# Kernel tuning notes

Hardware: AMD Instinct MI355X
Metric: run time of the kernel (lower is better)

## Reference

```python
import jax, jax.numpy as jnp
import numpy as np

N_NODES = 50000
N_EDGES = 800000
DIM = 128
N_LAYERS = 2          # num_layers - 1 GIN layers
NUM_GRAPHS = 512      # rows of the sparse graph_pool matrix
BN_EPS = 1e-5


def setup_inputs() -> dict:
    key = jax.random.key(0)
    ks = jax.random.split(key, 10)
    x = jax.random.normal(ks[0], (N_NODES, DIM), dtype=jnp.float32)
    edge_src = jax.random.randint(ks[1], (N_EDGES,), 0, N_NODES, dtype=jnp.int32)
    edge_dst = jax.random.randint(ks[2], (N_EDGES,), 0, N_NODES, dtype=jnp.int32)
    edge_weight = jax.random.uniform(ks[3], (N_EDGES,), dtype=jnp.float32)
    graph_ids = jnp.sort(jax.random.randint(ks[4], (N_NODES,), 0, NUM_GRAPHS, dtype=jnp.int32))
    pool_w = jnp.ones((N_NODES,), dtype=jnp.float32)
    scale = 1.0 / np.sqrt(DIM)
    W1 = jax.random.normal(ks[5], (N_LAYERS, DIM, DIM), dtype=jnp.float32) * scale
    b1 = jnp.zeros((N_LAYERS, DIM), dtype=jnp.float32)
    W2 = jax.random.normal(ks[6], (N_LAYERS, DIM, DIM), dtype=jnp.float32) * scale
    b2 = jnp.zeros((N_LAYERS, DIM), dtype=jnp.float32)
    bn_gamma = jnp.ones((N_LAYERS, DIM), dtype=jnp.float32)
    bn_beta = jnp.zeros((N_LAYERS, DIM), dtype=jnp.float32)
    return {"x": x, "edge_src": edge_src, "edge_dst": edge_dst,
            "edge_weight": edge_weight, "graph_ids": graph_ids, "pool_w": pool_w,
            "W1": W1, "b1": b1, "W2": W2, "b2": b2,
            "bn_gamma": bn_gamma, "bn_beta": bn_beta}


def reference(x, edge_src, edge_dst, edge_weight, graph_ids, pool_w,
              W1, b1, W2, b2, bn_gamma, bn_beta):
    h = x
    n = h.shape[0]
    for l in range(N_LAYERS):
        # pooled = adj @ h, adj in COO form: adj[dst, src] = edge_weight
        msg = edge_weight[:, None] * h[edge_src]                    # [E, D] gather
        pooled = jax.ops.segment_sum(msg, edge_dst, num_segments=n) # [N, D] scatter-add
        # 2-linear MLP (num_mlp_layers=2): Linear -> ReLU -> Linear
        hid = jax.nn.relu(pooled @ W1[l] + b1[l])
        z = hid @ W2[l] + b2[l]
        # BatchNorm1d over the node dimension (training-mode batch stats)
        mu = jnp.mean(z, axis=0)
        var = jnp.mean(jnp.square(z - mu), axis=0)
        z = bn_gamma[l] * (z - mu) * jax.lax.rsqrt(var + BN_EPS) + bn_beta[l]
        h = jax.nn.relu(z)
    x_nodes = h
    # pooled_x = graph_pool @ h, graph_pool[g, i] = pool_w[i] for node i in graph g
    pooled_x = jax.ops.segment_sum(pool_w[:, None] * h, graph_ids,
                                   num_segments=NUM_GRAPHS)
    return pooled_x, x_nodes
```

## Files before the change

kernel.cpp:

```cpp
#include <hip/hip_runtime.h>

#define N_NODES    50000
#define N_EDGES    800000
#define DIM        128
#define NUM_GRAPHS 512
#define BN_EPS     1e-5f

#define NBUCK      196
#define TILE       2048
#define MLP_ROWS   128
#define POOL_SPLIT 2

typedef unsigned int u32;
typedef unsigned short u16;
typedef __attribute__((ext_vector_type(8))) short bf16x8;
typedef __attribute__((ext_vector_type(4))) float f32x4;

__device__ __forceinline__ u16 f2bf(float f) {
    u32 u = __float_as_uint(f);
    u += 0x7FFF + ((u >> 16) & 1);
    return (u16)(u >> 16);
}
__device__ __forceinline__ float bf2f(u16 h) {
    return __uint_as_float((u32)h << 16);
}

__global__ __launch_bounds__(256)
void fill_zero_kernel(float* __restrict__ p, long long n)
{
    long long stride = (long long)gridDim.x * blockDim.x;
    for (long long i = blockIdx.x * 256LL + threadIdx.x; i < n; i += stride)
        p[i] = 0.f;
}

__global__ __launch_bounds__(256)
void cvt_bf16_kernel(const float* __restrict__ in, u16* __restrict__ out, long long n4)
{
    long long stride = (long long)gridDim.x * blockDim.x;
    for (long long i = blockIdx.x * 256LL + threadIdx.x; i < n4; i += stride) {
        float4 v = ((const float4*)in)[i];
        ushort4 o;
        o.x = f2bf(v.x); o.y = f2bf(v.y); o.z = f2bf(v.z); o.w = f2bf(v.w);
        ((ushort4*)out)[i] = o;
    }
}

__global__ __launch_bounds__(256)
void cvt_wt_kernel(const float* __restrict__ W1, const float* __restrict__ W2,
                   u16* __restrict__ wt)
{
    int idx = blockIdx.x * 256 + threadIdx.x;
    if (idx >= 4 * 128 * 128) return;
    int m    = idx >> 14;
    int f    = idx & 16383;
    int c    = (f >> 11) & 7;
    int kk   = (f >> 9) & 3;
    int lane = (f >> 3) & 63;
    int e    = f & 7;
    int k = kk * 32 + ((lane >> 4) << 3) + e;
    int j = c * 16 + (lane & 15);
    const float* src = (m & 1) ? W2 : W1;
    src += (m >> 1) * 128 * 128;
    wt[idx] = f2bf(src[k * 128 + j]);
}

__global__ __launch_bounds__(256)
void bucket_hist(const int* __restrict__ dst, int* __restrict__ bucketCnt)
{
    __shared__ int cnt[NBUCK];
    int t = threadIdx.x;
    if (t < NBUCK) cnt[t] = 0;
    __syncthreads();
    int stride = gridDim.x * blockDim.x;
    for (int e = blockIdx.x * 256 + t; e < N_EDGES; e += stride)
        atomicAdd(&cnt[dst[e] >> 8], 1);
    __syncthreads();
    if (t < NBUCK && cnt[t] > 0) atomicAdd(&bucketCnt[t], cnt[t]);
}

__global__ __launch_bounds__(256)
void bucket_scan(const int* __restrict__ bucketCnt, int* __restrict__ bucketStart,
                 int* __restrict__ gCursor)
{
    __shared__ int s[256];
    int t = threadIdx.x;
    int v = (t < NBUCK) ? bucketCnt[t] : 0;
    s[t] = v;
    __syncthreads();
    for (int off = 1; off < 256; off <<= 1) {
        int x = (t >= off) ? s[t - off] : 0;
        __syncthreads();
        s[t] += x;
        __syncthreads();
    }
    int excl = s[t] - v;
    if (t <= NBUCK) bucketStart[t] = excl;
    if (t < NBUCK)  gCursor[t] = excl;
}

__global__ __launch_bounds__(256)
void partitionA(const int* __restrict__ src, const int* __restrict__ dst,
                const float* __restrict__ ew, int* __restrict__ gCursor,
                uint2* __restrict__ ed2)
{
    __shared__ int cnt[NBUCK];
    __shared__ int off[NBUCK];
    __shared__ int gb[NBUCK];
    __shared__ u32 stg_sw[TILE];
    __shared__ u32 stg_d[TILE];
    __shared__ int scanb[256];

    const int t = threadIdx.x;
    const int base = blockIdx.x * TILE;
    const int tcnt = min(TILE, N_EDGES - base);

    if (t < NBUCK) cnt[t] = 0;
    __syncthreads();

    u32 swv[8], dv[8];
    int rk[8], bk[8];
    #pragma unroll
    for (int j = 0; j < 8; ++j) {
        int e = base + j * 256 + t;
        if (e < N_EDGES) {
            int d = dst[e];
            swv[j] = ((u32)f2bf(ew[e]) << 16) | (u32)src[e];
            dv[j]  = (u32)d;
            bk[j]  = d >> 8;
            rk[j]  = atomicAdd(&cnt[bk[j]], 1);
        } else bk[j] = -1;
    }
    __syncthreads();

    {
        int v = (t < NBUCK) ? cnt[t] : 0;
        scanb[t] = v;
        __syncthreads();
        for (int o = 1; o < 256; o <<= 1) {
            int x = (t >= o) ? scanb[t - o] : 0;
            __syncthreads();
            scanb[t] += x;
            __syncthreads();
        }
        if (t < NBUCK) off[t] = scanb[t] - v;
    }
    __syncthreads();

    #pragma unroll
    for (int j = 0; j < 8; ++j) {
        if (bk[j] >= 0) {
            int idx = off[bk[j]] + rk[j];
            stg_sw[idx] = swv[j];
            stg_d[idx]  = dv[j];
        }
    }
    if (t < NBUCK && cnt[t] > 0) gb[t] = atomicAdd(&gCursor[t], cnt[t]);
    __syncthreads();

    for (int j = t; j < tcnt; j += 256) {
        u32 d = stg_d[j];
        int b = (int)(d >> 8);
        int pos = gb[b] + (j - off[b]);
        ed2[pos] = make_uint2(stg_sw[j], d);
    }
}

__global__ __launch_bounds__(256)
void partitionB(const uint2* __restrict__ ed2, const int* __restrict__ bucketStart,
                int* __restrict__ rowptr, u32* __restrict__ ed)
{
    __shared__ int hist[256];
    __shared__ int sc[256];
    __shared__ int cur[256];

    const int b = blockIdx.x;
    const int t = threadIdx.x;
    const int s = bucketStart[b];
    const int n = bucketStart[b + 1] - s;

    hist[t] = 0;
    __syncthreads();
    for (int j = t; j < n; j += 256)
        atomicAdd(&hist[ed2[s + j].y & 255u], 1);
    __syncthreads();

    int v = hist[t];
    sc[t] = v;
    __syncthreads();
    for (int o = 1; o < 256; o <<= 1) {
        int x = (t >= o) ? sc[t - o] : 0;
        __syncthreads();
        sc[t] += x;
        __syncthreads();
    }
    int excl = sc[t] - v;
    rowptr[b * 256 + t] = s + excl;
    cur[t] = s + excl;
    __syncthreads();

    for (int j = t; j < n; j += 256) {
        uint2 r = ed2[s + j];
        int d = (int)(r.y & 255u);
        int p = atomicAdd(&cur[d], 1);
        ed[p] = r.x;
    }
}

template<bool BN>
__global__ __launch_bounds__(256)
void gather_spmm(const u16* __restrict__ h, const u32* __restrict__ ed,
                 const int* __restrict__ rowptr, u16* __restrict__ pooled,
                 const float* __restrict__ stats, const float* __restrict__ gamma,
                 const float* __restrict__ beta)
{
    __shared__ float scs[128];
    __shared__ float shs[128];
    if (BN) {
        if (threadIdx.x < 128) {
            int c = threadIdx.x;
            float mu  = stats[c] * (1.f / N_NODES);
            float var = stats[128 + c] * (1.f / N_NODES) - mu * mu;
            float s   = gamma[c] * rsqrtf(var + BN_EPS);
            scs[c] = s;
            shs[c] = beta[c] - mu * s;
        }
        __syncthreads();
    }

    int node = blockIdx.x * 16 + (threadIdx.x >> 4);
    int lane = threadIdx.x & 15;
    int beg = rowptr[node];
    int end = rowptr[node + 1];

    float sc8[8], sh8[8];
    if (BN) {
        #pragma unroll
        for (int q = 0; q < 8; ++q) {
            sc8[q] = scs[lane * 8 + q];
            sh8[q] = shs[lane * 8 + q];
        }
    }

    float acc[8];
    #pragma unroll
    for (int q = 0; q < 8; ++q) acc[q] = 0.f;

    for (int base = beg; base < end; base += 16) {
        int e = base + lane;
        u32 sw = (e < end) ? ed[e] : 0u;
        int cnt = min(16, end - base);
        #pragma unroll 4
        for (int i = 0; i < cnt; ++i) {
            u32 rec = __shfl(sw, i, 16);
            int   s = (int)(rec & 0xFFFFu);
            float w = bf2f((u16)(rec >> 16));
            bf16x8 hv = *((const bf16x8*)(h + (long long)s * DIM) + lane);
            #pragma unroll
            for (int q = 0; q < 8; ++q) {
                float v = bf2f((u16)hv[q]);
                if (BN) v = fmaxf(v * sc8[q] + sh8[q], 0.f);
                acc[q] += w * v;
            }
        }
    }
    bf16x8 o;
    #pragma unroll
    for (int q = 0; q < 8; ++q) o[q] = (short)f2bf(acc[q]);
    *((bf16x8*)(pooled + (long long)node * DIM) + lane) = o;
}

__global__ __launch_bounds__(512)
void fused_mlp(const u16* __restrict__ A, const u16* __restrict__ wtL,
               const float* __restrict__ b1, const float* __restrict__ b2,
               u16* __restrict__ Z, float* __restrict__ stats)
{
    __shared__ __align__(16) u16 wfrag[32768];
    __shared__ float ssum[128];
    __shared__ float ssq[128];

    const int tid  = threadIdx.x;
    const int lane = tid & 63;
    const int wave = tid >> 6;
    const int l15  = lane & 15;
    const int lk   = lane >> 4;
    const int row0 = blockIdx.x * MLP_ROWS;
    const int wrow = wave * 16;

    #pragma unroll
    for (int i = 0; i < 8; ++i) {
        int idx = tid + i * 512;
        *(bf16x8*)&wfrag[idx * 8] = *(const bf16x8*)(wtL + idx * 8);
    }
    if (tid < 128) { ssum[tid] = 0.f; ssq[tid] = 0.f; }

    bf16x8 afr[4];
    {
        int rg = row0 + wrow + l15;
        bool ok = rg < N_NODES;
        const u16* ap = A + (long long)rg * 128 + lk * 8;
        bf16x8 zero = {};
        #pragma unroll
        for (int kk = 0; kk < 4; ++kk)
            afr[kk] = ok ? *(const bf16x8*)(ap + kk * 32) : zero;
    }
    __syncthreads();

    f32x4 acc1[8];
    #pragma unroll
    for (int c = 0; c < 8; ++c) {
        float bv = b1[c * 16 + l15];
        f32x4 a = {bv, bv, bv, bv};
        #pragma unroll
        for (int kk = 0; kk < 4; ++kk) {
            bf16x8 w = *(bf16x8*)&wfrag[((c * 4 + kk) * 64 + lane) * 8];
            a = __builtin_amdgcn_mfma_f32_16x16x32_bf16(afr[kk], w, a, 0, 0, 0);
        }
        acc1[c] = a;
    }
    __syncthreads();

    #pragma unroll
    for (int c = 0; c < 8; ++c) {
        #pragma unroll
        for (int i = 0; i < 4; ++i) {
            int row = wrow + lk * 4 + i;
            int col = c * 16 + l15;
            wfrag[row * 128 + (col ^ ((row & 15) << 3))] = f2bf(fmaxf(acc1[c][i], 0.f));
        }
    }

    bf16x8 afr2[4];
    {
        int row = wrow + l15;
        #pragma unroll
        for (int kk = 0; kk < 4; ++kk)
            afr2[kk] = *(bf16x8*)&wfrag[row * 128 + ((kk * 32 + lk * 8) ^ ((row & 15) << 3))];
    }

    #pragma unroll
    for (int c = 0; c < 8; ++c) {
        float bv = b2[c * 16 + l15];
        f32x4 a = {bv, bv, bv, bv};
        #pragma unroll
        for (int kk = 0; kk < 4; ++kk) {
            bf16x8 w = *(bf16x8*)&wfrag[16384 + ((c * 4 + kk) * 64 + lane) * 8];
            a = __builtin_amdgcn_mfma_f32_16x16x32_bf16(afr2[kk], w, a, 0, 0, 0);
        }
        float s = 0.f, sq = 0.f;
        #pragma unroll
        for (int i = 0; i < 4; ++i) {
            int row = wrow + lk * 4 + i;
            int rg  = row0 + row;
            float v = a[i];
            bool ok = rg < N_NODES;
            if (ok) { s += v; sq += v * v; }
            wfrag[row * 128 + ((c * 16 + l15) ^ ((row & 15) << 3))] = ok ? f2bf(v) : (u16)0;
        }
        s  += __shfl_xor(s, 16);  s  += __shfl_xor(s, 32);
        sq += __shfl_xor(sq, 16); sq += __shfl_xor(sq, 32);
        if (lk == 0) {
            atomicAdd(&ssum[c * 16 + l15], s);
            atomicAdd(&ssq[c * 16 + l15], sq);
        }
    }

    #pragma unroll
    for (int j = 0; j < 4; ++j) {
        int chunk = j * 64 + lane;
        int rl  = chunk >> 4;
        int c8  = chunk & 15;
        int row = wrow + rl;
        int rg  = row0 + row;
        if (rg < N_NODES) {
            bf16x8 v = *(bf16x8*)&wfrag[row * 128 + ((c8 * 8) ^ ((row & 15) << 3))];
            *(bf16x8*)(Z + (long long)rg * 128 + c8 * 8) = v;
        }
    }
    __syncthreads();
    if (tid < 128) {
        atomicAdd(&stats[tid], ssum[tid]);
        atomicAdd(&stats[128 + tid], ssq[tid]);
    }
}

__global__ __launch_bounds__(256)
void graph_pool_bn(const u16* __restrict__ z, const float* __restrict__ stats,
                   const float* __restrict__ gamma, const float* __restrict__ beta,
                   const int* __restrict__ gid, const float* __restrict__ pw,
                   float* __restrict__ out_nodes, float* __restrict__ out_pool)
{
    __shared__ float scs[128];
    __shared__ float shs[128];
    if (threadIdx.x < 128) {
        int c = threadIdx.x;
        float mu  = stats[c] * (1.f / N_NODES);
        float var = stats[128 + c] * (1.f / N_NODES) - mu * mu;
        float s   = gamma[c] * rsqrtf(var + BN_EPS);
        scs[c] = s;
        shs[c] = beta[c] - mu * s;
    }
    __syncthreads();

    int g    = blockIdx.x >> 1;
    int half = blockIdx.x & 1;

    int lo = 0, hi = N_NODES;
    while (lo < hi) { int m = (lo + hi) >> 1; if (gid[m] < g) lo = m + 1; else hi = m; }
    int start = lo;
    hi = N_NODES;
    while (lo < hi) { int m = (lo + hi) >> 1; if (gid[m] < g + 1) lo = m + 1; else hi = m; }
    int end = lo;

    int len = end - start;
    int hlen = (len + 1) >> 1;
    int s = start + half * hlen;
    int e = min(end, s + hlen);

    const int t  = threadIdx.x;
    const int rg = t >> 5;
    const int c4 = t & 31;
    float4 sc4 = *(float4*)&scs[c4 * 4];
    float4 sh4 = *(float4*)&shs[c4 * 4];

    float4 acc = make_float4(0.f, 0.f, 0.f, 0.f);
    for (int r = s + rg; r < e; r += 8) {
        float w = pw[r];
        ushort4 hv = *((const ushort4*)(z + (long long)r * DIM) + c4);
        float4 v;
        v.x = fmaxf(bf2f(hv.x) * sc4.x + sh4.x, 0.f);
        v.y = fmaxf(bf2f(hv.y) * sc4.y + sh4.y, 0.f);
        v.z = fmaxf(bf2f(hv.z) * sc4.z + sh4.z, 0.f);
        v.w = fmaxf(bf2f(hv.w) * sc4.w + sh4.w, 0.f);
        *((float4*)(out_nodes + (long long)r * DIM) + c4) = v;
        acc.x += w * v.x; acc.y += w * v.y;
        acc.z += w * v.z; acc.w += w * v.w;
    }

    __shared__ float4 sd[256];
    sd[t] = acc;
    __syncthreads();
    if (t < 32) {
        float4 tot = sd[t];
        #pragma unroll
        for (int i = 1; i < 8; ++i) {
            float4 v = sd[i * 32 + t];
            tot.x += v.x; tot.y += v.y; tot.z += v.z; tot.w += v.w;
        }
        float* op = out_pool + g * DIM + t * 4;
        atomicAdd(op + 0, tot.x);
        atomicAdd(op + 1, tot.y);
        atomicAdd(op + 2, tot.z);
        atomicAdd(op + 3, tot.w);
    }
}

extern "C" void kernel_launch(void* const* d_in, const int* in_sizes, int n_in,
                              void* d_out, int out_size, void* d_ws, size_t ws_size,
                              hipStream_t stream)
{
    const float* x    = (const float*)d_in[0];
    const int*   esrc = (const int*)d_in[1];
    const int*   edst = (const int*)d_in[2];
    const float* ew   = (const float*)d_in[3];
    const int*   gid  = (const int*)d_in[4];
    const float* pw   = (const float*)d_in[5];
    const float* W1   = (const float*)d_in[6];
    const float* b1   = (const float*)d_in[7];
    const float* W2   = (const float*)d_in[8];
    const float* b2   = (const float*)d_in[9];
    const float* gam  = (const float*)d_in[10];
    const float* bet  = (const float*)d_in[11];

    float* out_pool  = (float*)d_out;
    float* out_nodes = (float*)d_out + NUM_GRAPHS * DIM;

    const size_t NF = (size_t)N_NODES * DIM;
    char* w = (char*)d_ws;
    uint2* ed2      = (uint2*)w;      w += (size_t)N_EDGES * sizeof(uint2);
    u32*   ed       = (u32*)w;        w += (size_t)N_EDGES * sizeof(u32);
    u16*   pooledBf = (u16*)w;        w += NF * sizeof(u16);
    u16*   zBf      = (u16*)w;        w += NF * sizeof(u16);
    u16*   hx       = (u16*)w;        w += NF * sizeof(u16);
    u16*   wt       = (u16*)w;        w += (size_t)4 * 128 * 128 * sizeof(u16);
    float* stats0   = (float*)w;      w += 256 * sizeof(float);
    float* stats1   = (float*)w;      w += 256 * sizeof(float);
    int*   bucketCnt= (int*)w;        w += 256 * sizeof(int);
    int*   bucketStart=(int*)w;       w += 256 * sizeof(int);
    int*   gCursor  = (int*)w;        w += 256 * sizeof(int);
    int*   rowptr   = (int*)w;        w += (NBUCK * 256 + 64) * sizeof(int);

    const int mlpGrid    = (N_NODES + MLP_ROWS - 1) / MLP_ROWS;
    const int gatherGrid = (N_NODES + 15) / 16;
    const int partGrid   = (N_EDGES + TILE - 1) / TILE;

    fill_zero_kernel<<<1, 256, 0, stream>>>(stats0, 768);
    fill_zero_kernel<<<64, 256, 0, stream>>>(out_pool, NUM_GRAPHS * DIM);
    bucket_hist<<<512, 256, 0, stream>>>(edst, bucketCnt);
    cvt_bf16_kernel<<<1024, 256, 0, stream>>>(x, hx, (long long)(NF / 4));
    cvt_wt_kernel<<<256, 256, 0, stream>>>(W1, W2, wt);
    bucket_scan<<<1, 256, 0, stream>>>(bucketCnt, bucketStart, gCursor);
    partitionA<<<partGrid, 256, 0, stream>>>(esrc, edst, ew, gCursor, ed2);
    partitionB<<<NBUCK, 256, 0, stream>>>(ed2, bucketStart, rowptr, ed);

    gather_spmm<false><<<gatherGrid, 256, 0, stream>>>(hx, ed, rowptr, pooledBf,
                                                       nullptr, nullptr, nullptr);
    fused_mlp<<<mlpGrid, 512, 0, stream>>>(pooledBf, wt, b1, b2, zBf, stats0);

    gather_spmm<true><<<gatherGrid, 256, 0, stream>>>(zBf, ed, rowptr, pooledBf,
                                                      stats0, gam, bet);
    fused_mlp<<<mlpGrid, 512, 0, stream>>>(pooledBf, wt + 32768,
                                           b1 + DIM, b2 + DIM, zBf, stats1);

    graph_pool_bn<<<NUM_GRAPHS * POOL_SPLIT, 256, 0, stream>>>(
        zBf, stats1, gam + DIM, bet + DIM, gid, pw, out_nodes, out_pool);
}
```

Measured before the change: 183.6 us.

## Merge zero-fill launches, vectorize histogram, enlarge partition tiles, prefetch edge records

Several independent tweaks: the two zero-fill kernels become one launch, the bucket histogram reads dst as int4, and partitionA uses 4096-edge tiles with 512 threads. The gather kernel prefetches the next chunk of edge records, and graph pooling splits each graph four ways. Together these aim to cut launch overhead, raise memory-level parallelism and improve load balance, at the cost of more shared memory per partition block and more atomics into out_pool.

```diff
diff --git a/kernel.cpp b/kernel.cpp
--- a/kernel.cpp
+++ b/kernel.cpp
@@ -7,9 +7,9 @@
 #define BN_EPS     1e-5f
 
 #define NBUCK      196
-#define TILE       2048
+#define TILE       4096
 #define MLP_ROWS   128
-#define POOL_SPLIT 2
+#define POOL_SPLIT 4
 
 typedef unsigned int u32;
 typedef unsigned short u16;
@@ -26,11 +26,13 @@
 }
 
 __global__ __launch_bounds__(256)
-void fill_zero_kernel(float* __restrict__ p, long long n)
-{
-    long long stride = (long long)gridDim.x * blockDim.x;
-    for (long long i = blockIdx.x * 256LL + threadIdx.x; i < n; i += stride)
-        p[i] = 0.f;
+void fill_zero2_kernel(float* __restrict__ p1, int n1, float* __restrict__ p2, int n2)
+{
+    int stride = gridDim.x * blockDim.x;
+    for (int i = blockIdx.x * 256 + threadIdx.x; i < n1 + n2; i += stride) {
+        if (i < n1) p1[i] = 0.f;
+        else        p2[i - n1] = 0.f;
+    }
 }
 
 __global__ __launch_bounds__(256)
@@ -72,8 +74,13 @@
     if (t < NBUCK) cnt[t] = 0;
     __syncthreads();
     int stride = gridDim.x * blockDim.x;
-    for (int e = blockIdx.x * 256 + t; e < N_EDGES; e += stride)
-        atomicAdd(&cnt[dst[e] >> 8], 1);
+    for (int i = blockIdx.x * 256 + t; i < N_EDGES / 4; i += stride) {
+        int4 d = ((const int4*)dst)[i];
+        atomicAdd(&cnt[d.x >> 8], 1);
+        atomicAdd(&cnt[d.y >> 8], 1);
+        atomicAdd(&cnt[d.z >> 8], 1);
+        atomicAdd(&cnt[d.w >> 8], 1);
+    }
     __syncthreads();
     if (t < NBUCK && cnt[t] > 0) atomicAdd(&bucketCnt[t], cnt[t]);
 }
@@ -98,7 +105,7 @@
     if (t < NBUCK)  gCursor[t] = excl;
 }
 
-__global__ __launch_bounds__(256)
+__global__ __launch_bounds__(512)
 void partitionA(const int* __restrict__ src, const int* __restrict__ dst,
                 const float* __restrict__ ew, int* __restrict__ gCursor,
                 uint2* __restrict__ ed2)
@@ -121,7 +128,7 @@
     int rk[8], bk[8];
     #pragma unroll
     for (int j = 0; j < 8; ++j) {
-        int e = base + j * 256 + t;
+        int e = base + j * 512 + t;
         if (e < N_EDGES) {
             int d = dst[e];
             swv[j] = ((u32)f2bf(ew[e]) << 16) | (u32)src[e];
@@ -134,12 +141,12 @@
 
     {
         int v = (t < NBUCK) ? cnt[t] : 0;
-        scanb[t] = v;
+        if (t < 256) scanb[t] = v;
         __syncthreads();
         for (int o = 1; o < 256; o <<= 1) {
-            int x = (t >= o) ? scanb[t - o] : 0;
+            int x = (t < 256 && t >= o) ? scanb[t - o] : 0;
             __syncthreads();
-            scanb[t] += x;
+            if (t < 256) scanb[t] += x;
             __syncthreads();
         }
         if (t < NBUCK) off[t] = scanb[t] - v;
@@ -157,7 +164,7 @@
     if (t < NBUCK && cnt[t] > 0) gb[t] = atomicAdd(&gCursor[t], cnt[t]);
     __syncthreads();
 
-    for (int j = t; j < tcnt; j += 256) {
+    for (int j = t; j < tcnt; j += 512) {
         u32 d = stg_d[j];
         int b = (int)(d >> 8);
         int pos = gb[b] + (j - off[b]);
@@ -245,16 +252,16 @@
     #pragma unroll
     for (int q = 0; q < 8; ++q) acc[q] = 0.f;
 
+    u32 sw_cur = (beg + lane < end) ? ed[beg + lane] : 0u;
     for (int base = beg; base < end; base += 16) {
-        int e = base + lane;
-        u32 sw = (e < end) ? ed[e] : 0u;
+        u32 sw_next = (base + 16 + lane < end) ? ed[base + 16 + lane] : 0u;
         int cnt = min(16, end - base);
         #pragma unroll 4
         for (int i = 0; i < cnt; ++i) {
-            u32 rec = __shfl(sw, i, 16);
-            int   s = (int)(rec & 0xFFFFu);
+            u32 rec = __shfl(sw_cur, i, 16);
+            long long s = (long long)(rec & 0xFFFFu);
             float w = bf2f((u16)(rec >> 16));
-            bf16x8 hv = *((const bf16x8*)(h + (long long)s * DIM) + lane);
+            bf16x8 hv = *((const bf16x8*)(h + (s << 7)) + lane);
             #pragma unroll
             for (int q = 0; q < 8; ++q) {
                 float v = bf2f((u16)hv[q]);
@@ -262,11 +269,12 @@
                 acc[q] += w * v;
             }
         }
+        sw_cur = sw_next;
     }
     bf16x8 o;
     #pragma unroll
     for (int q = 0; q < 8; ++q) o[q] = (short)f2bf(acc[q]);
-    *((bf16x8*)(pooled + (long long)node * DIM) + lane) = o;
+    *((bf16x8*)(pooled + ((long long)node << 7)) + lane) = o;
 }
 
 __global__ __launch_bounds__(512)
@@ -401,8 +409,8 @@
     }
     __syncthreads();
 
-    int g    = blockIdx.x >> 1;
-    int half = blockIdx.x & 1;
+    int g    = blockIdx.x >> 2;
+    int part = blockIdx.x & 3;
 
     int lo = 0, hi = N_NODES;
     while (lo < hi) { int m = (lo + hi) >> 1; if (gid[m] < g) lo = m + 1; else hi = m; }
@@ -411,10 +419,10 @@
     while (lo < hi) { int m = (lo + hi) >> 1; if (gid[m] < g + 1) lo = m + 1; else hi = m; }
     int end = lo;
 
-    int len = end - start;
-    int hlen = (len + 1) >> 1;
-    int s = start + half * hlen;
-    int e = min(end, s + hlen);
+    int len  = end - start;
+    int qlen = (len + 3) >> 2;
+    int s = start + part * qlen;
+    int e = min(end, s + qlen);
 
     const int t  = threadIdx.x;
     const int rg = t >> 5;
@@ -493,13 +501,13 @@
     const int gatherGrid = (N_NODES + 15) / 16;
     const int partGrid   = (N_EDGES + TILE - 1) / TILE;
 
-    fill_zero_kernel<<<1, 256, 0, stream>>>(stats0, 768);
-    fill_zero_kernel<<<64, 256, 0, stream>>>(out_pool, NUM_GRAPHS * DIM);
-    bucket_hist<<<512, 256, 0, stream>>>(edst, bucketCnt);
+    fill_zero2_kernel<<<64, 256, 0, stream>>>(stats0, 768,
+                                              out_pool, NUM_GRAPHS * DIM);
+    bucket_hist<<<256, 256, 0, stream>>>(edst, bucketCnt);
     cvt_bf16_kernel<<<1024, 256, 0, stream>>>(x, hx, (long long)(NF / 4));
     cvt_wt_kernel<<<256, 256, 0, stream>>>(W1, W2, wt);
     bucket_scan<<<1, 256, 0, stream>>>(bucketCnt, bucketStart, gCursor);
-    partitionA<<<partGrid, 256, 0, stream>>>(esrc, edst, ew, gCursor, ed2);
+    partitionA<<<partGrid, 512, 0, stream>>>(esrc, edst, ew, gCursor, ed2);
     partitionB<<<NBUCK, 256, 0, stream>>>(ed2, bucketStart, rowptr, ed);
 
     gather_spmm<false><<<gatherGrid, 256, 0, stream>>>(hx, ed, rowptr, pooledBf,
```

Result: faster. 173.5 us (-5.5%).
